# Performance work log

Hardware: AMD Instinct MI355X
Metric: run time of the kernel (lower is better)

## Reference

```python
import jax, jax.numpy as jnp
import numpy as np

B, N, M, F, D, OUT = 2, 8192, 8192, 128, 3, 512

def setup_inputs() -> dict:
    key = jax.random.key(0)
    k1, k2, k3, k4, k5 = jax.random.split(key, 5)
    return {
        'geometry': jax.random.normal(k1, (B, N, D), dtype=jnp.float32),
        'gaussian_pcd': jax.random.normal(k2, (B, M, D), dtype=jnp.float32),
        'features': jax.random.normal(k3, (B, M, F), dtype=jnp.float32),
        'W_proj': jax.random.normal(k4, (OUT, F), dtype=jnp.float32) / np.sqrt(F),
        'b_proj': jax.random.normal(k5, (OUT,), dtype=jnp.float32) * 0.01,
        'k': 10,
    }

def reference(geometry, gaussian_pcd, features, W_proj, b_proj, k):
    # cdist via ||q||^2 + ||p||^2 - 2 q.p (matches torch.cdist matmul mode)
    q2 = jnp.sum(geometry * geometry, axis=-1)            # [B,N]
    p2 = jnp.sum(gaussian_pcd * gaussian_pcd, axis=-1)    # [B,M]
    d2 = q2[:, :, None] + p2[:, None, :] - 2.0 * jnp.einsum('bnd,bmd->bnm', geometry, gaussian_pcd)
    dists = jnp.sqrt(jnp.maximum(d2, 0.0))                # [B,N,M]
    # k smallest, sorted ascending
    neg_d, idx = jax.lax.top_k(-dists, k)                 # [B,N,k]
    knn_d = -neg_d
    # gather knn features: [B,N,k,F]
    knn_f = jax.vmap(lambda f, i: f[i])(features, idx)
    # inverse-distance weights, normalized
    w = 1.0 / (knn_d + 1e-8)
    w = w / jnp.sum(w, axis=-1, keepdims=True)
    interp = jnp.einsum('bnk,bnkf->bnf', w, knn_f)        # [B,N,F]
    # gaussian_feature_proj: Linear(128 -> feature_dim)
    return jnp.einsum('bnf,of->bno', interp, W_proj) + b_proj
```

## Files before the change

### kernel.cpp

```cpp
#include <hip/hip_runtime.h>
#include <math.h>

#define NQ   8192
#define NP   8192
#define NF   128
#define NOUT 512
#define NB   2
#define KNN  10
#define BNQ  (NB*NQ)
#define QW   2

typedef unsigned long long u64;
typedef unsigned short ushort_t;
typedef __attribute__((ext_vector_type(8))) short bf16x8;
typedef __attribute__((ext_vector_type(4))) float f32x4;

__device__ __forceinline__ u64 shfl64(u64 v, int src) {
  unsigned lo = (unsigned)__shfl((int)(unsigned)(v & 0xffffffffull), src, 64);
  unsigned hi = (unsigned)__shfl((int)(unsigned)(v >> 32), src, 64);
  return ((u64)hi << 32) | lo;
}
__device__ __forceinline__ u64 shflup64(u64 v) {
  unsigned lo = (unsigned)__shfl_up((int)(unsigned)(v & 0xffffffffull), 1, 64);
  unsigned hi = (unsigned)__shfl_up((int)(unsigned)(v >> 32), 1, 64);
  return ((u64)hi << 32) | lo;
}

__device__ __forceinline__ float dist2s(float m2x, float m2y, float m2z,
                                        float4 p) {
  return fmaf(m2x, p.x, fmaf(m2y, p.y, fmaf(m2z, p.z, p.w)));
}

__device__ __forceinline__ unsigned fmono(float f) {
  unsigned u = __float_as_uint(f);
  return u ^ ((unsigned)((int)u >> 31) | 0x80000000u);
}

__device__ __forceinline__ float nextupf(float f) {
  unsigned u = __float_as_uint(f);
  unsigned n = (u & 0x80000000u) ? ((u == 0x80000000u) ? 1u : u - 1u) : u + 1u;
  return __uint_as_float(n);
}

__device__ __forceinline__ float wmin64f(float v) {
#pragma unroll
  for (int off = 1; off < 64; off <<= 1)
    v = fminf(v, __shfl_xor(v, off, 64));
  return v;
}

__device__ __forceinline__ ushort_t f2bf(float x) {
  unsigned u = __float_as_uint(x);
  return (ushort_t)((u + 0x7FFFu + ((u >> 16) & 1u)) >> 16);
}

__global__ __launch_bounds__(256) void prep_kernel(
    const float* __restrict__ gpcd, const float* __restrict__ W,
    float4* __restrict__ pts4, ushort_t* __restrict__ Wb)
{
  int tid = blockIdx.x * 256 + threadIdx.x;
  if (tid < NB * NP) {
    const float* p = gpcd + (size_t)tid * 3;
    float x = p[0], y = p[1], z = p[2];
    float p2 = x * x + y * y + z * z;
    pts4[tid] = make_float4(x, y, z, p2);
  }
  Wb[tid] = f2bf(W[tid]);
}

__global__ __launch_bounds__(256) void knn_interp_kernel(
    const float* __restrict__ geometry, const float4* __restrict__ pts4,
    const float* __restrict__ features, ushort_t* __restrict__ Abf)
{
  const int lane = threadIdx.x & 63;
  const int wave = (blockIdx.x << 2) | (threadIdx.x >> 6);
  const int q0   = wave * QW;
  const int b    = q0 >> 13;
  const float4* __restrict__ P = pts4 + ((size_t)b << 13);

  float m2x[QW], m2y[QW], m2z[QW], q2[QW];
#pragma unroll
  for (int j = 0; j < QW; ++j) {
    const float* g = geometry + (size_t)(q0 + j) * 3;
    float x = g[0], y = g[1], z = g[2];
    q2[j]  = x * x + y * y + z * z;
    m2x[j] = -2.0f * x; m2y[j] = -2.0f * y; m2z[j] = -2.0f * z;
  }

  float lmin[QW];
#pragma unroll
  for (int j = 0; j < QW; ++j) lmin[j] = INFINITY;
#pragma unroll 2
  for (int t = 0; t < NP / 64; ++t) {
    const float4 p = P[(t << 6) | lane];
#pragma unroll
    for (int j = 0; j < QW; ++j)
      lmin[j] = fminf(lmin[j], dist2s(m2x[j], m2y[j], m2z[j], p));
  }

  float theta[QW];
#pragma unroll
  for (int j = 0; j < QW; ++j) {
    float lm  = lmin[j];
    float tau = 0.0f;
#pragma unroll
    for (int r = 0; r < KNN; ++r) {
      tau = wmin64f(lm);
      u64 mk = __ballot(lm == tau);
      int w  = __builtin_ctzll(mk);
      if (lane == w) lm = INFINITY;
    }
    theta[j] = nextupf(tau);
  }

  u64   list[QW];
  float dl[QW];
#pragma unroll
  for (int j = 0; j < QW; ++j) {
    list[j] = 0xFFFFFFFFFFFFFFFFull;
    dl[j]   = INFINITY;
  }
  const float qnan = __builtin_nanf("");

  for (int t = 0; t < NP / 64; ++t) {
    const float4 p = P[(t << 6) | lane];
#pragma unroll
    for (int j = 0; j < QW; ++j) {
      float d2 = dist2s(m2x[j], m2y[j], m2z[j], p);
      for (;;) {
        u64 mask = __ballot(d2 < theta[j]);
        if (!mask) break;
        int src = __builtin_ctzll(mask);
        float cd = __uint_as_float(
            (unsigned)__builtin_amdgcn_readlane(__float_as_int(d2), src));
        u64 kk = ((u64)fmono(cd) << 32) | (unsigned)((t << 6) + src);
        u64   prev  = shflup64(list[j]);
        float prevd = __shfl(dl[j], lane - 1, 64);
        bool mylt = list[j] < kk;
        bool pins = (lane == 0) || (prev < kk);
        list[j] = mylt ? list[j] : (pins ? kk : prev);
        dl[j]   = mylt ? dl[j]  : (pins ? cd : prevd);
        theta[j] = fminf(theta[j], __uint_as_float(
            (unsigned)__builtin_amdgcn_readlane(__float_as_int(dl[j]), 9)));
        if (lane == src) d2 = qnan;
      }
    }
  }

  const float* __restrict__ F = features + (size_t)b * NP * NF;
#pragma unroll
  for (int j = 0; j < QW; ++j) {
    float td2 = fmaxf(dl[j] + q2[j], 0.0f);
    float w   = 1.0f / (sqrtf(td2) + 1e-8f);
    float wsum = 0.0f;
#pragma unroll
    for (int jj = 0; jj < KNN; ++jj) wsum += __shfl(w, jj, 64);

    float a0 = 0.0f, a1 = 0.0f;
#pragma unroll
    for (int jj = 0; jj < KNN; ++jj) {
      float wj = __shfl(w, jj, 64) / wsum;
      int  mi  = (int)(unsigned)(shfl64(list[j], jj) & 0xffffffffull);
      const float2 f2 = *(const float2*)(F + (size_t)mi * NF + (lane << 1));
      a0 = fmaf(wj, f2.x, a0);
      a1 = fmaf(wj, f2.y, a1);
    }
    unsigned pack = (unsigned)f2bf(a0) | ((unsigned)f2bf(a1) << 16);
    *(unsigned*)(Abf + (size_t)(q0 + j) * NF + (lane << 1)) = pack;
  }
}

__global__ __launch_bounds__(256) void proj_mfma(
    const ushort_t* __restrict__ Abf, const ushort_t* __restrict__ Wb,
    const float* __restrict__ bias, float* __restrict__ out)
{
  const int lane = threadIdx.x & 63;
  const int w    = threadIdx.x >> 6;
  const int mt   = blockIdx.x & 127;
  const int ot   = blockIdx.x >> 7;
  const int m0   = (mt << 7) + ((w & 1) << 6);
  const int o0   = (ot << 6) + ((w >> 1) << 5);
  const int r    = lane & 15;
  const int kg   = (lane >> 4) << 3;

  f32x4 acc[4][2];
#pragma unroll
  for (int i = 0; i < 4; ++i)
#pragma unroll
    for (int jn = 0; jn < 2; ++jn) acc[i][jn] = (f32x4)0.0f;

#pragma unroll
  for (int ks = 0; ks < 4; ++ks) {
    const int k0 = (ks << 5) + kg;
    bf16x8 a[4], bb[2];
#pragma unroll
    for (int i = 0; i < 4; ++i)
      a[i] = *(const bf16x8*)(Abf + (size_t)(m0 + (i << 4) + r) * NF + k0);
#pragma unroll
    for (int jn = 0; jn < 2; ++jn)
      bb[jn] = *(const bf16x8*)(Wb + (size_t)(o0 + (jn << 4) + r) * NF + k0);
#pragma unroll
    for (int i = 0; i < 4; ++i)
#pragma unroll
      for (int jn = 0; jn < 2; ++jn)
        acc[i][jn] = __builtin_amdgcn_mfma_f32_16x16x32_bf16(
            a[i], bb[jn], acc[i][jn], 0, 0, 0);
  }

  const int crow = (lane >> 4) << 2;
#pragma unroll
  for (int jn = 0; jn < 2; ++jn) {
    const int oc = o0 + (jn << 4) + r;
    const float bv = bias[oc];
#pragma unroll
    for (int i = 0; i < 4; ++i) {
#pragma unroll
      for (int reg = 0; reg < 4; ++reg) {
        const int qm = m0 + (i << 4) + crow + reg;
        out[(size_t)qm * NOUT + oc] = acc[i][jn][reg] + bv;
      }
    }
  }
}

extern "C" void kernel_launch(void* const* d_in, const int* in_sizes, int n_in,
                              void* d_out, int out_size, void* d_ws, size_t ws_size,
                              hipStream_t stream) {
  const float* geometry = (const float*)d_in[0];
  const float* gpcd     = (const float*)d_in[1];
  const float* features = (const float*)d_in[2];
  const float* W        = (const float*)d_in[3];
  const float* bias     = (const float*)d_in[4];
  float* out = (float*)d_out;

  char*     ws   = (char*)d_ws;
  ushort_t* Abf  = (ushort_t*)ws;
  float4*   pts4 = (float4*)(ws + (size_t)BNQ * NF * 2);
  ushort_t* Wb   = (ushort_t*)(ws + (size_t)BNQ * NF * 2 + (size_t)NB * NP * 16);

  prep_kernel<<<256, 256, 0, stream>>>(gpcd, W, pts4, Wb);
  knn_interp_kernel<<<BNQ / (QW * 4), 256, 0, stream>>>(geometry, pts4, features, Abf);
  proj_mfma<<<(BNQ / 128) * (NOUT / 64), 256, 0, stream>>>(Abf, Wb, bias, out);
}
```

Before: 112.3 us.

## Stage point chunks in LDS with register-prefetched double buffering for KNN scans

Both passes over the candidate points in the KNN kernel now read from a 1024-point chunk held in shared memory. The block cooperatively loads the next chunk into registers while the current chunk is scanned, then writes it to LDS between barriers. This replaces per-wave global/L2 loads of all points, which were repeated by every wave, with one cooperative load per block. The cost is extra block-level barriers, which force the divergent ballot-insert loop of all four waves to synchronize per chunk.

```diff
diff --git a/kernel.cpp b/kernel.cpp
--- a/kernel.cpp
+++ b/kernel.cpp
@@ -9,6 +9,7 @@
 #define KNN  10
 #define BNQ  (NB*NQ)
 #define QW   2
+#define CH   1024
 
 typedef unsigned long long u64;
 typedef unsigned short ushort_t;
@@ -72,11 +73,14 @@
     const float* __restrict__ geometry, const float4* __restrict__ pts4,
     const float* __restrict__ features, ushort_t* __restrict__ Abf)
 {
+  __shared__ __align__(16) float4 Pl[CH];
+
   const int lane = threadIdx.x & 63;
   const int wave = (blockIdx.x << 2) | (threadIdx.x >> 6);
   const int q0   = wave * QW;
   const int b    = q0 >> 13;
   const float4* __restrict__ P = pts4 + ((size_t)b << 13);
+  const int tid4 = threadIdx.x << 2;
 
   float m2x[QW], m2y[QW], m2z[QW], q2[QW];
 #pragma unroll
@@ -87,15 +91,43 @@
     m2x[j] = -2.0f * x; m2y[j] = -2.0f * y; m2z[j] = -2.0f * z;
   }
 
+  float4 st0, st1, st2, st3;
+
+  {
+    const float4* s = P + tid4;
+    st0 = s[0]; st1 = s[1]; st2 = s[2]; st3 = s[3];
+    float4* d = &Pl[tid4];
+    d[0] = st0; d[1] = st1; d[2] = st2; d[3] = st3;
+  }
+  __syncthreads();
+
   float lmin[QW];
 #pragma unroll
   for (int j = 0; j < QW; ++j) lmin[j] = INFINITY;
-#pragma unroll 2
-  for (int t = 0; t < NP / 64; ++t) {
-    const float4 p = P[(t << 6) | lane];
-#pragma unroll
-    for (int j = 0; j < QW; ++j)
-      lmin[j] = fminf(lmin[j], dist2s(m2x[j], m2y[j], m2z[j], p));
+
+  for (int c = 0; c < NP / CH; ++c) {
+    if (c < NP / CH - 1) {
+      const float4* s = P + ((c + 1) << 10) + tid4;
+      st0 = s[0]; st1 = s[1]; st2 = s[2]; st3 = s[3];
+    }
+#pragma unroll
+    for (int i = 0; i < CH / 64; ++i) {
+      const float4 p = Pl[(i << 6) + lane];
+#pragma unroll
+      for (int j = 0; j < QW; ++j)
+        lmin[j] = fminf(lmin[j], dist2s(m2x[j], m2y[j], m2z[j], p));
+    }
+    __syncthreads();
+    if (c < NP / CH - 1) {
+      float4* d = &Pl[tid4];
+      d[0] = st0; d[1] = st1; d[2] = st2; d[3] = st3;
+      __syncthreads();
+    }
+  }
+
+  {
+    const float4* s = P + tid4;
+    st0 = s[0]; st1 = s[1]; st2 = s[2]; st3 = s[3];
   }
 
   float theta[QW];
@@ -122,28 +154,48 @@
   }
   const float qnan = __builtin_nanf("");
 
-  for (int t = 0; t < NP / 64; ++t) {
-    const float4 p = P[(t << 6) | lane];
-#pragma unroll
-    for (int j = 0; j < QW; ++j) {
-      float d2 = dist2s(m2x[j], m2y[j], m2z[j], p);
-      for (;;) {
-        u64 mask = __ballot(d2 < theta[j]);
-        if (!mask) break;
-        int src = __builtin_ctzll(mask);
-        float cd = __uint_as_float(
-            (unsigned)__builtin_amdgcn_readlane(__float_as_int(d2), src));
-        u64 kk = ((u64)fmono(cd) << 32) | (unsigned)((t << 6) + src);
-        u64   prev  = shflup64(list[j]);
-        float prevd = __shfl(dl[j], lane - 1, 64);
-        bool mylt = list[j] < kk;
-        bool pins = (lane == 0) || (prev < kk);
-        list[j] = mylt ? list[j] : (pins ? kk : prev);
-        dl[j]   = mylt ? dl[j]  : (pins ? cd : prevd);
-        theta[j] = fminf(theta[j], __uint_as_float(
-            (unsigned)__builtin_amdgcn_readlane(__float_as_int(dl[j]), 9)));
-        if (lane == src) d2 = qnan;
+  {
+    float4* d = &Pl[tid4];
+    d[0] = st0; d[1] = st1; d[2] = st2; d[3] = st3;
+  }
+  __syncthreads();
+
+  for (int c = 0; c < NP / CH; ++c) {
+    if (c < NP / CH - 1) {
+      const float4* s = P + ((c + 1) << 10) + tid4;
+      st0 = s[0]; st1 = s[1]; st2 = s[2]; st3 = s[3];
+    }
+#pragma unroll 4
+    for (int i = 0; i < CH / 64; ++i) {
+      const float4 p = Pl[(i << 6) + lane];
+      const int ib = (c << 10) + (i << 6);
+#pragma unroll
+      for (int j = 0; j < QW; ++j) {
+        float d2 = dist2s(m2x[j], m2y[j], m2z[j], p);
+        for (;;) {
+          u64 mask = __ballot(d2 < theta[j]);
+          if (!mask) break;
+          int src = __builtin_ctzll(mask);
+          float cd = __uint_as_float(
+              (unsigned)__builtin_amdgcn_readlane(__float_as_int(d2), src));
+          u64 kk = ((u64)fmono(cd) << 32) | (unsigned)(ib + src);
+          u64   prev  = shflup64(list[j]);
+          float prevd = __shfl(dl[j], lane - 1, 64);
+          bool mylt = list[j] < kk;
+          bool pins = (lane == 0) || (prev < kk);
+          list[j] = mylt ? list[j] : (pins ? kk : prev);
+          dl[j]   = mylt ? dl[j]  : (pins ? cd : prevd);
+          theta[j] = fminf(theta[j], __uint_as_float(
+              (unsigned)__builtin_amdgcn_readlane(__float_as_int(dl[j]), 9)));
+          if (lane == src) d2 = qnan;
+        }
       }
+    }
+    __syncthreads();
+    if (c < NP / CH - 1) {
+      float4* d = &Pl[tid4];
+      d[0] = st0; d[1] = st1; d[2] = st2; d[3] = st3;
+      __syncthreads();
     }
   }
 
```

New measurement: 121.8 us. 8.4% more time.

## Buffer KNN candidates in LDS and batch-insert into sorted list

Applied to the files above, without the earlier changes.

Instead of running the serial per-candidate insertion loop as soon as any lane passes the threshold, candidates that beat the threshold are compacted with ballot and popcount into a per-wave shared-memory buffer of 64 entries. The buffer is drained through the sorted-list insertion loop only when it would overflow and once more at the end. The aim is to cut per-iteration ballot/shuffle overhead and divergence in the second scan. The cost is that the threshold tightens less often, so more candidates may be buffered and inserted, and the kernel now uses LDS.

```diff
diff --git a/kernel.cpp b/kernel.cpp
--- a/kernel.cpp
+++ b/kernel.cpp
@@ -9,8 +9,10 @@
 #define KNN  10
 #define BNQ  (NB*NQ)
 #define QW   2
+#define CAP  64
 
 typedef unsigned long long u64;
+typedef unsigned int u32;
 typedef unsigned short ushort_t;
 typedef __attribute__((ext_vector_type(8))) short bf16x8;
 typedef __attribute__((ext_vector_type(4))) float f32x4;
@@ -35,7 +37,6 @@
   unsigned u = __float_as_uint(f);
   return u ^ ((unsigned)((int)u >> 31) | 0x80000000u);
 }
-
 __device__ __forceinline__ float nextupf(float f) {
   unsigned u = __float_as_uint(f);
   unsigned n = (u & 0x80000000u) ? ((u == 0x80000000u) ? 1u : u - 1u) : u + 1u;
@@ -47,6 +48,29 @@
   for (int off = 1; off < 64; off <<= 1)
     v = fminf(v, __shfl_xor(v, off, 64));
   return v;
+}
+
+__device__ __forceinline__ void insert_loop(float d2, int idxv, int lane,
+                                            u64& lst, float& dlv, float& th) {
+  for (;;) {
+    u64 mask = __ballot(d2 < th);
+    if (!mask) break;
+    int src = __builtin_ctzll(mask);
+    float cd = __uint_as_float(
+        (unsigned)__builtin_amdgcn_readlane(__float_as_int(d2), src));
+    int  ci = __builtin_amdgcn_readlane(idxv, src);
+    u64 kk = ((u64)fmono(cd) << 32) | (u32)ci;
+    u64   prev  = shflup64(lst);
+    float prevd = __shfl(dlv, lane - 1, 64);
+    bool mylt = lst < kk;
+    bool pins = (lane == 0) || (prev < kk);
+    lst = mylt ? lst : (pins ? kk : prev);
+    dlv = mylt ? dlv : (pins ? cd : prevd);
+    float d9 = __uint_as_float(
+        (unsigned)__builtin_amdgcn_readlane(__float_as_int(dlv), 9));
+    th = fminf(th, nextupf(d9));
+    if (lane == src) d2 = __builtin_nanf("");
+  }
 }
 
 __device__ __forceinline__ ushort_t f2bf(float x) {
@@ -72,8 +96,12 @@
     const float* __restrict__ geometry, const float4* __restrict__ pts4,
     const float* __restrict__ features, ushort_t* __restrict__ Abf)
 {
+  __shared__ float cdL[4][QW][CAP];
+  __shared__ int   ciL[4][QW][CAP];
+
   const int lane = threadIdx.x & 63;
-  const int wave = (blockIdx.x << 2) | (threadIdx.x >> 6);
+  const int wb   = threadIdx.x >> 6;
+  const int wave = (blockIdx.x << 2) | wb;
   const int q0   = wave * QW;
   const int b    = q0 >> 13;
   const float4* __restrict__ P = pts4 + ((size_t)b << 13);
@@ -98,7 +126,7 @@
       lmin[j] = fminf(lmin[j], dist2s(m2x[j], m2y[j], m2z[j], p));
   }
 
-  float theta[QW];
+  float th[QW];
 #pragma unroll
   for (int j = 0; j < QW; ++j) {
     float lm  = lmin[j];
@@ -107,45 +135,62 @@
     for (int r = 0; r < KNN; ++r) {
       tau = wmin64f(lm);
       u64 mk = __ballot(lm == tau);
-      int w  = __builtin_ctzll(mk);
+      int w = __builtin_ctzll(mk);
       if (lane == w) lm = INFINITY;
     }
-    theta[j] = nextupf(tau);
+    th[j] = nextupf(tau);
   }
 
   u64   list[QW];
   float dl[QW];
-#pragma unroll
-  for (int j = 0; j < QW; ++j) {
-    list[j] = 0xFFFFFFFFFFFFFFFFull;
-    dl[j]   = INFINITY;
+  int   count[QW];
+#pragma unroll
+  for (int j = 0; j < QW; ++j) {
+    list[j]  = 0xFFFFFFFFFFFFFFFFull;
+    dl[j]    = INFINITY;
+    count[j] = 0;
   }
   const float qnan = __builtin_nanf("");
+
+  auto finalize = [&](int j) {
+    for (int base2 = 0; base2 < count[j]; base2 += 64) {
+      const int sidx = base2 + lane;
+      float cd2 = qnan;
+      int   cid = 0;
+      if (sidx < count[j]) { cd2 = cdL[wb][j][sidx]; cid = ciL[wb][j][sidx]; }
+      insert_loop(cd2, cid, lane, list[j], dl[j], th[j]);
+    }
+    count[j] = 0;
+  };
 
   for (int t = 0; t < NP / 64; ++t) {
     const float4 p = P[(t << 6) | lane];
+    const int  idx = (t << 6) | lane;
 #pragma unroll
     for (int j = 0; j < QW; ++j) {
-      float d2 = dist2s(m2x[j], m2y[j], m2z[j], p);
-      for (;;) {
-        u64 mask = __ballot(d2 < theta[j]);
-        if (!mask) break;
-        int src = __builtin_ctzll(mask);
-        float cd = __uint_as_float(
-            (unsigned)__builtin_amdgcn_readlane(__float_as_int(d2), src));
-        u64 kk = ((u64)fmono(cd) << 32) | (unsigned)((t << 6) + src);
-        u64   prev  = shflup64(list[j]);
-        float prevd = __shfl(dl[j], lane - 1, 64);
-        bool mylt = list[j] < kk;
-        bool pins = (lane == 0) || (prev < kk);
-        list[j] = mylt ? list[j] : (pins ? kk : prev);
-        dl[j]   = mylt ? dl[j]  : (pins ? cd : prevd);
-        theta[j] = fminf(theta[j], __uint_as_float(
-            (unsigned)__builtin_amdgcn_readlane(__float_as_int(dl[j]), 9)));
-        if (lane == src) d2 = qnan;
+      const float d2 = dist2s(m2x[j], m2y[j], m2z[j], p);
+      const bool hit = d2 < th[j];
+      const u64 mask = __ballot(hit);
+      if (!mask) continue;
+      const int pc = __popcll(mask);
+      if (count[j] + pc > CAP) {
+        finalize(j);
+        float d2m = hit ? d2 : qnan;
+        insert_loop(d2m, idx, lane, list[j], dl[j], th[j]);
+      } else {
+        if (hit) {
+          const int slot = count[j] +
+              (int)__popcll(mask & ((1ull << lane) - 1ull));
+          cdL[wb][j][slot] = d2;
+          ciL[wb][j][slot] = idx;
+        }
+        count[j] += pc;
       }
     }
   }
+
+#pragma unroll
+  for (int j = 0; j < QW; ++j) finalize(j);
 
   const float* __restrict__ F = features + (size_t)b * NP * NF;
 #pragma unroll
@@ -160,7 +205,7 @@
 #pragma unroll
     for (int jj = 0; jj < KNN; ++jj) {
       float wj = __shfl(w, jj, 64) / wsum;
-      int  mi  = (int)(unsigned)(shfl64(list[j], jj) & 0xffffffffull);
+      int  mi  = (int)(u32)(shfl64(list[j], jj) & 0xffffffffull);
       const float2 f2 = *(const float2*)(F + (size_t)mi * NF + (lane << 1));
       a0 = fmaf(wj, f2.x, a0);
       a1 = fmaf(wj, f2.y, a1);
```

Measured after the change: 107.7 us. 1.04x faster.
